# Kernel tuning notes

Measured on AMD Instinct MI355X. Metric: run time of the kernel, lower is better.

The kernel has to match this reference:

```python
import jax, jax.numpy as jnp
import numpy as np
import math

N = 8192  # base points
M = 8192  # target points
FEAT = 5
DESC = 4
HID = 32


def setup_inputs() -> dict:
    key = jax.random.key(0)
    ks = jax.random.split(key, 16)
    s = lambda fan_in: 1.0 / np.sqrt(fan_in)
    return {
        "base_pos": jax.random.normal(ks[0], (N, 2), jnp.float32),
        "base_feat": jax.random.normal(ks[1], (N, FEAT), jnp.float32),
        "base_desc": jax.random.normal(ks[2], (DESC,), jnp.float32),
        "target_pos": jax.random.normal(ks[3], (M, 2), jnp.float32),
        "target_feat": jax.random.normal(ks[4], (M, FEAT), jnp.float32),
        "target_desc": jax.random.normal(ks[5], (DESC,), jnp.float32),
        # NodeWeightNet MLP params (Linear(5,32) -> ReLU -> Linear(32,1))
        "w1": jax.random.uniform(ks[6], (FEAT, HID), jnp.float32, -s(FEAT), s(FEAT)),
        "b1": jax.random.uniform(ks[7], (HID,), jnp.float32, -s(FEAT), s(FEAT)),
        "w2": jax.random.uniform(ks[8], (HID, 1), jnp.float32, -s(HID), s(HID)),
        "b2": jax.random.uniform(ks[9], (1,), jnp.float32, -s(HID), s(HID)),
        # descriptor gate params (Linear(4,32) -> ReLU -> Linear(32,1))
        "g1": jax.random.uniform(ks[10], (DESC, HID), jnp.float32, -s(DESC), s(DESC)),
        "gb1": jax.random.uniform(ks[11], (HID,), jnp.float32, -s(DESC), s(DESC)),
        "g2": jax.random.uniform(ks[12], (HID, 1), jnp.float32, -s(HID), s(HID)),
        "gb2": jax.random.uniform(ks[13], (1,), jnp.float32, -s(HID), s(HID)),
        "log_sigma": jnp.asarray(math.log(0.1), jnp.float32),
        "log_scale": jnp.zeros((2,), jnp.float32),
        "bias": jnp.zeros((1,), jnp.float32),
    }


def _node_weights(feat, w1, b1, w2, b2):
    logits = jax.nn.relu(feat @ w1 + b1) @ w2 + b2  # [N,1]
    w = jax.nn.softplus(logits) + 1e-6
    return (w / w.sum())[:, 0]  # [N], sums to 1


def _mmd_term(x, wx, y, wy, inv_two_sigma2):
    # weighted sum of Gaussian kernel over all pairs, via sq-dist expansion
    d2 = (
        (x * x).sum(-1)[:, None]
        + (y * y).sum(-1)[None, :]
        - 2.0 * (x @ y.T)
    )
    k = jnp.exp(-d2 * inv_two_sigma2)
    return jnp.einsum("i,ij,j->", wx, k, wy)


def reference(base_pos, base_feat, base_desc, target_pos, target_feat, target_desc,
              w1, b1, w2, b2, g1, gb1, g2, gb2, log_sigma, log_scale, bias):
    scale = jnp.exp(log_scale)
    bp = base_pos * scale
    tp = target_pos * scale
    sigma = jnp.exp(log_sigma)
    bw = _node_weights(base_feat, w1, b1, w2, b2)
    tw = _node_weights(target_feat, w1, b1, w2, b2)
    # center=True: subtract each cloud's weighted mean
    bp = bp - (bw[:, None] * bp).sum(0)
    tp = tp - (tw[:, None] * tp).sum(0)
    inv = 1.0 / (2.0 * sigma * sigma)
    loss = (
        _mmd_term(bp, bw, bp, bw, inv)
        - 2.0 * _mmd_term(bp, bw, tp, tw, inv)
        + _mmd_term(tp, tw, tp, tw, inv)
    )
    diff = jnp.abs(base_desc - target_desc)  # [4]
    gate = jax.nn.softplus(jax.nn.relu(diff @ g1 + gb1) @ g2 + gb2) + 1e-6  # [1]
    return loss * gate.squeeze() + bias.squeeze()
```

## Files before the change

kernel.cpp:

```cpp
#include <hip/hip_runtime.h>
#include <math.h>


#define WK_THREADS 256
#define MMD_THREADS 256
#define IB 256
#define JB 256
#define NPART 16

__device__ __forceinline__ float softplusf(float x) {
    return fmaxf(x, 0.0f) + log1pf(expf(-fabsf(x)));
}

__device__ __forceinline__ float fast_exp2(float x) {
#if __has_builtin(__builtin_amdgcn_exp2f)
    return __builtin_amdgcn_exp2f(x);
#else
    return exp2f(x);
#endif
}

__global__ __launch_bounds__(WK_THREADS) void weight_kernel(
    const float* __restrict__ bpos, const float* __restrict__ bfeat,
    const float* __restrict__ tpos, const float* __restrict__ tfeat,
    const float* __restrict__ w1, const float* __restrict__ b1,
    const float* __restrict__ w2, const float* __restrict__ b2,
    const float* __restrict__ log_sigma, const float* __restrict__ log_scale,
    float4* __restrict__ b4, float4* __restrict__ t4,
    float* __restrict__ sums, int n, int m)
{
    int idx = blockIdx.x * WK_THREADS + threadIdx.x;
    int total = n + m;
    float w = 0.f, px = 0.f, py = 0.f;
    int cloud = 0;
    if (idx < total) {
        const float* pos; const float* feat; int i;
        if (idx < n) { pos = bpos; feat = bfeat; i = idx; cloud = 0; }
        else         { pos = tpos; feat = tfeat; i = idx - n; cloud = 1; }
        float sigma = expf(log_sigma[0]);
        float u = 0.8493218003f / sigma;
        float sx = expf(log_scale[0]) * u;
        float sy = expf(log_scale[1]) * u;
        px = pos[2*i]   * sx;
        py = pos[2*i+1] * sy;
        float f0 = feat[5*i], f1 = feat[5*i+1], f2 = feat[5*i+2],
              f3 = feat[5*i+3], f4 = feat[5*i+4];
        float logit = b2[0];
        #pragma unroll
        for (int h = 0; h < 32; ++h) {
            float a = b1[h];
            a = fmaf(f0, w1[h],      a);
            a = fmaf(f1, w1[32+h],   a);
            a = fmaf(f2, w1[64+h],   a);
            a = fmaf(f3, w1[96+h],   a);
            a = fmaf(f4, w1[128+h],  a);
            a = fmaxf(a, 0.f);
            logit = fmaf(a, w2[h], logit);
        }
        w = softplusf(logit) + 1e-6f;
        float4 v = make_float4(px, py, w, 0.f);
        if (cloud == 0) b4[i] = v; else t4[i] = v;
    }
    float sw = w, swx = w*px, swy = w*py;
    #pragma unroll
    for (int off = 32; off > 0; off >>= 1) {
        sw  += __shfl_down(sw,  off, 64);
        swx += __shfl_down(swx, off, 64);
        swy += __shfl_down(swy, off, 64);
    }
    if ((threadIdx.x & 63) == 0 && idx < total) {
        float* dst = sums + 3 + cloud * 3;
        atomicAdd(dst + 0, sw);
        atomicAdd(dst + 1, swx);
        atomicAdd(dst + 2, swy);
    }
}

__global__ __launch_bounds__(MMD_THREADS) void mmd_kernel(
    const float4* __restrict__ b4, const float4* __restrict__ t4,
    const float* __restrict__ sums, float* __restrict__ partial,
    int n, int m)
{
    int t = blockIdx.z;
    const float4* X; const float4* Y; int nx, ny;
    if (t == 0)      { X = b4; Y = b4; nx = n; ny = n; }
    else if (t == 1) { X = b4; Y = t4; nx = n; ny = m; }
    else             { X = t4; Y = t4; nx = m; ny = m; }

    int ibase = blockIdx.x * IB;
    int j0 = blockIdx.y * JB;
    if (ibase >= nx || j0 >= ny) return;

    float dx0 = 0.f, dy0 = 0.f;
    if (t == 1) {
        float sb = sums[3], st = sums[6];
        dx0 = sums[4] / sb - sums[7] / st;
        dy0 = sums[5] / sb - sums[8] / st;
    }

    int i = ibase + threadIdx.x;
    float xi = 0.f, yi = 0.f, wi = 0.f;
    if (i < nx) {
        float4 v = X[i];
        xi = v.x - dx0; yi = v.y - dy0; wi = v.z;
    }

    int jn = min(JB, ny - j0);
    const float4* Yp = Y + j0;
    float acc = 0.f;
    for (int j = 0; j < jn; ++j) {
        float4 q = Yp[j];
        float dx = xi - q.x;
        float dy = yi - q.y;
        float e = fast_exp2(fmaf(dy, -dy, -(dx * dx)));
        acc = fmaf(q.z, e, acc);
    }
    float r = wi * acc;

    #pragma unroll
    for (int off = 32; off > 0; off >>= 1) r += __shfl_down(r, off, 64);
    __shared__ float wsum[MMD_THREADS / 64];
    int wid = threadIdx.x >> 6;
    if ((threadIdx.x & 63) == 0) wsum[wid] = r;
    __syncthreads();
    if (threadIdx.x == 0) {
        float tot = 0.f;
        #pragma unroll
        for (int k = 0; k < MMD_THREADS / 64; ++k) tot += wsum[k];
        atomicAdd(&partial[t * NPART + (blockIdx.x & (NPART - 1))], tot);
    }
}

__global__ void final_kernel(
    const float* __restrict__ bdesc, const float* __restrict__ tdesc,
    const float* __restrict__ g1, const float* __restrict__ gb1,
    const float* __restrict__ g2, const float* __restrict__ gb2,
    const float* __restrict__ bias, const float* __restrict__ sums,
    const float* __restrict__ partial, float* __restrict__ out)
{
    if (threadIdx.x != 0 || blockIdx.x != 0) return;
    float P[3];
    #pragma unroll
    for (int t = 0; t < 3; ++t) {
        float s = 0.f;
        #pragma unroll
        for (int k = 0; k < NPART; ++k) s += partial[t * NPART + k];
        P[t] = s;
    }
    float sb = sums[3], st = sums[6];
    float loss = P[0] / (sb * sb) - 2.f * P[1] / (sb * st) + P[2] / (st * st);

    float d0 = fabsf(bdesc[0] - tdesc[0]);
    float d1 = fabsf(bdesc[1] - tdesc[1]);
    float d2 = fabsf(bdesc[2] - tdesc[2]);
    float d3 = fabsf(bdesc[3] - tdesc[3]);
    float logit = gb2[0];
    #pragma unroll
    for (int h = 0; h < 32; ++h) {
        float a = gb1[h];
        a = fmaf(d0, g1[h],      a);
        a = fmaf(d1, g1[32+h],   a);
        a = fmaf(d2, g1[64+h],   a);
        a = fmaf(d3, g1[96+h],   a);
        a = fmaxf(a, 0.f);
        logit = fmaf(a, g2[h], logit);
    }
    float gate = softplusf(logit) + 1e-6f;
    out[0] = loss * gate + bias[0];
}

extern "C" void kernel_launch(void* const* d_in, const int* in_sizes, int n_in,
                              void* d_out, int out_size, void* d_ws, size_t ws_size,
                              hipStream_t stream)
{
    const float* bpos      = (const float*)d_in[0];
    const float* bfeat     = (const float*)d_in[1];
    const float* bdesc     = (const float*)d_in[2];
    const float* tpos      = (const float*)d_in[3];
    const float* tfeat     = (const float*)d_in[4];
    const float* tdesc     = (const float*)d_in[5];
    const float* w1        = (const float*)d_in[6];
    const float* b1        = (const float*)d_in[7];
    const float* w2        = (const float*)d_in[8];
    const float* b2        = (const float*)d_in[9];
    const float* g1        = (const float*)d_in[10];
    const float* gb1       = (const float*)d_in[11];
    const float* g2        = (const float*)d_in[12];
    const float* gb2       = (const float*)d_in[13];
    const float* log_sigma = (const float*)d_in[14];
    const float* log_scale = (const float*)d_in[15];
    const float* bias      = (const float*)d_in[16];
    float* out = (float*)d_out;

    int n = in_sizes[0] / 2;
    int m = in_sizes[3] / 2;

    char* ws = (char*)d_ws;
    float4* b4   = (float4*)ws;
    float4* t4   = (float4*)(ws + (size_t)n * sizeof(float4));
    float* sums  = (float*)(ws + (size_t)(n + m) * sizeof(float4));
    float* partial = sums + 9;

    hipMemsetAsync(sums, 0, (9 + 3 * NPART) * sizeof(float), stream);

    int total = n + m;
    int wb = (total + WK_THREADS - 1) / WK_THREADS;
    weight_kernel<<<wb, WK_THREADS, 0, stream>>>(
        bpos, bfeat, tpos, tfeat, w1, b1, w2, b2, log_sigma, log_scale,
        b4, t4, sums, n, m);

    int nmax = n > m ? n : m;
    dim3 grid((nmax + IB - 1) / IB, (nmax + JB - 1) / JB, 3);
    mmd_kernel<<<grid, MMD_THREADS, 0, stream>>>(b4, t4, sums, partial, n, m);

    final_kernel<<<1, 64, 0, stream>>>(bdesc, tdesc, g1, gb1, g2, gb2,
                                       bias, sums, partial, out);
}
```

Baseline: 157.4 us.

## Register-block MMD pairs, stage Y tile in LDS, drop atomics and memset

Each MMD thread now handles four i-points against an LDS-staged tile of 128 j-points. The squared distance is expanded as -|x|^2 - |y|^2 + 2x·y, with the per-point norm precomputed in the weight kernel, so each pair costs about three FMAs plus one exp2. Atomic accumulation and the memset are replaced by per-wave and per-block partial slots that are reduced deterministically in the cross-term blocks and in a wider final kernel. The MLP weights are cached in LDS. The trade-off is that every cross-term block redundantly reduces the weight partials, and the expansion form can lose some precision for distant points.

```diff
diff --git a/kernel.cpp b/kernel.cpp
--- a/kernel.cpp
+++ b/kernel.cpp
@@ -4,9 +4,9 @@
 
 #define WK_THREADS 256
 #define MMD_THREADS 256
-#define IB 256
-#define JB 256
-#define NPART 16
+#define I_PT 4
+#define IB (MMD_THREADS * I_PT)
+#define JB 128
 
 __device__ __forceinline__ float softplusf(float x) {
     return fmaxf(x, 0.0f) + log1pf(expf(-fabsf(x)));
@@ -27,9 +27,15 @@
     const float* __restrict__ w2, const float* __restrict__ b2,
     const float* __restrict__ log_sigma, const float* __restrict__ log_scale,
     float4* __restrict__ b4, float4* __restrict__ t4,
-    float* __restrict__ sums, int n, int m)
-{
-    int idx = blockIdx.x * WK_THREADS + threadIdx.x;
+    float* __restrict__ wpart, int n, int m)
+{
+    __shared__ float s_w1[160], s_b1[32], s_w2[32];
+    int tid = threadIdx.x;
+    if (tid < 160) s_w1[tid] = w1[tid];
+    if (tid < 32) { s_b1[tid] = b1[tid]; s_w2[tid] = w2[tid]; }
+    __syncthreads();
+
+    int idx = blockIdx.x * WK_THREADS + tid;
     int total = n + m;
     float w = 0.f, px = 0.f, py = 0.f;
     int cloud = 0;
@@ -48,38 +54,73 @@
         float logit = b2[0];
         #pragma unroll
         for (int h = 0; h < 32; ++h) {
-            float a = b1[h];
-            a = fmaf(f0, w1[h],      a);
-            a = fmaf(f1, w1[32+h],   a);
-            a = fmaf(f2, w1[64+h],   a);
-            a = fmaf(f3, w1[96+h],   a);
-            a = fmaf(f4, w1[128+h],  a);
+            float a = s_b1[h];
+            a = fmaf(f0, s_w1[h],      a);
+            a = fmaf(f1, s_w1[32+h],   a);
+            a = fmaf(f2, s_w1[64+h],   a);
+            a = fmaf(f3, s_w1[96+h],   a);
+            a = fmaf(f4, s_w1[128+h],  a);
             a = fmaxf(a, 0.f);
-            logit = fmaf(a, w2[h], logit);
+            logit = fmaf(a, s_w2[h], logit);
         }
         w = softplusf(logit) + 1e-6f;
-        float4 v = make_float4(px, py, w, 0.f);
+        float h_i = -fmaf(px, px, py * py);
+        float4 v = make_float4(px, py, h_i, w);
         if (cloud == 0) b4[i] = v; else t4[i] = v;
     }
-    float sw = w, swx = w*px, swy = w*py;
+    float sw = w, swx = w * px, swy = w * py;
     #pragma unroll
     for (int off = 32; off > 0; off >>= 1) {
         sw  += __shfl_down(sw,  off, 64);
         swx += __shfl_down(swx, off, 64);
         swy += __shfl_down(swy, off, 64);
     }
-    if ((threadIdx.x & 63) == 0 && idx < total) {
-        float* dst = sums + 3 + cloud * 3;
-        atomicAdd(dst + 0, sw);
-        atomicAdd(dst + 1, swx);
-        atomicAdd(dst + 2, swy);
-    }
+    if ((tid & 63) == 0) {
+        int wgid = blockIdx.x * (WK_THREADS / 64) + (tid >> 6);
+        float* dst = wpart + wgid * 6;
+        bool valid = (idx < total);
+        float z = valid ? 1.f : 0.f;
+        if (cloud == 0) {
+            dst[0] = sw * z; dst[1] = swx * z; dst[2] = swy * z;
+            dst[3] = 0.f;    dst[4] = 0.f;     dst[5] = 0.f;
+        } else {
+            dst[0] = 0.f;    dst[1] = 0.f;     dst[2] = 0.f;
+            dst[3] = sw * z; dst[4] = swx * z; dst[5] = swy * z;
+        }
+    }
+}
+
+__device__ __forceinline__ void reduce_wpart(const float* __restrict__ wpart,
+                                             int nslots, float out[6])
+{
+    __shared__ float lds6[4][6];
+    float v[6];
+    #pragma unroll
+    for (int k = 0; k < 6; ++k) v[k] = 0.f;
+    for (int s = threadIdx.x; s < nslots; s += blockDim.x) {
+        #pragma unroll
+        for (int k = 0; k < 6; ++k) v[k] += wpart[s * 6 + k];
+    }
+    #pragma unroll
+    for (int off = 32; off > 0; off >>= 1) {
+        #pragma unroll
+        for (int k = 0; k < 6; ++k) v[k] += __shfl_down(v[k], off, 64);
+    }
+    if ((threadIdx.x & 63) == 0) {
+        #pragma unroll
+        for (int k = 0; k < 6; ++k) lds6[threadIdx.x >> 6][k] = v[k];
+    }
+    __syncthreads();
+    #pragma unroll
+    for (int k = 0; k < 6; ++k)
+        out[k] = lds6[0][k] + lds6[1][k] + lds6[2][k] + lds6[3][k];
+    __syncthreads();
 }
 
 __global__ __launch_bounds__(MMD_THREADS) void mmd_kernel(
     const float4* __restrict__ b4, const float4* __restrict__ t4,
-    const float* __restrict__ sums, float* __restrict__ partial,
-    int n, int m)
+    const float* __restrict__ wpart, int nwslots,
+    float* __restrict__ partial, int n, int m, int gx, int gy)
 {
     int t = blockIdx.z;
     const float4* X; const float4* Y; int nx, ny;
@@ -87,86 +128,128 @@
     else if (t == 1) { X = b4; Y = t4; nx = n; ny = m; }
     else             { X = t4; Y = t4; nx = m; ny = m; }
 
+    int slot = (t * gy + blockIdx.y) * gx + blockIdx.x;
     int ibase = blockIdx.x * IB;
     int j0 = blockIdx.y * JB;
-    if (ibase >= nx || j0 >= ny) return;
+    if (ibase >= nx || j0 >= ny) {
+        if (threadIdx.x == 0) partial[slot] = 0.f;
+        return;
+    }
 
     float dx0 = 0.f, dy0 = 0.f;
     if (t == 1) {
-        float sb = sums[3], st = sums[6];
-        dx0 = sums[4] / sb - sums[7] / st;
-        dy0 = sums[5] / sb - sums[8] / st;
-    }
-
-    int i = ibase + threadIdx.x;
-    float xi = 0.f, yi = 0.f, wi = 0.f;
-    if (i < nx) {
-        float4 v = X[i];
-        xi = v.x - dx0; yi = v.y - dy0; wi = v.z;
+        float o[6];
+        reduce_wpart(wpart, nwslots, o);
+        dx0 = o[1] / o[0] - o[4] / o[3];
+        dy0 = o[2] / o[0] - o[5] / o[3];
+    }
+
+    __shared__ float4 ytile[JB];
+    if (threadIdx.x < JB) {
+        int jj = j0 + threadIdx.x;
+        ytile[threadIdx.x] = (jj < ny) ? Y[jj] : make_float4(0.f, 0.f, 0.f, 0.f);
+    }
+    __syncthreads();
+
+    float x2[I_PT], y2[I_PT], hi_[I_PT], wi[I_PT], acc[I_PT];
+    #pragma unroll
+    for (int s = 0; s < I_PT; ++s) {
+        int ii = ibase + s * MMD_THREADS + threadIdx.x;
+        float4 v = (ii < nx) ? X[ii] : make_float4(0.f, 0.f, 0.f, 0.f);
+        float xc = v.x - dx0, yc = v.y - dy0;
+        x2[s] = xc + xc;
+        y2[s] = yc + yc;
+        hi_[s] = -fmaf(xc, xc, yc * yc);
+        wi[s] = v.w;
+        acc[s] = 0.f;
     }
 
     int jn = min(JB, ny - j0);
-    const float4* Yp = Y + j0;
-    float acc = 0.f;
+    #pragma unroll 2
     for (int j = 0; j < jn; ++j) {
-        float4 q = Yp[j];
-        float dx = xi - q.x;
-        float dy = yi - q.y;
-        float e = fast_exp2(fmaf(dy, -dy, -(dx * dx)));
-        acc = fmaf(q.z, e, acc);
-    }
-    float r = wi * acc;
+        float4 q = ytile[j];
+        #pragma unroll
+        for (int s = 0; s < I_PT; ++s) {
+            float u = hi_[s] + q.z;
+            u = fmaf(x2[s], q.x, u);
+            u = fmaf(y2[s], q.y, u);
+            acc[s] = fmaf(q.w, fast_exp2(u), acc[s]);
+        }
+    }
+    float r = 0.f;
+    #pragma unroll
+    for (int s = 0; s < I_PT; ++s) r = fmaf(wi[s], acc[s], r);
 
     #pragma unroll
     for (int off = 32; off > 0; off >>= 1) r += __shfl_down(r, off, 64);
     __shared__ float wsum[MMD_THREADS / 64];
-    int wid = threadIdx.x >> 6;
-    if ((threadIdx.x & 63) == 0) wsum[wid] = r;
+    if ((threadIdx.x & 63) == 0) wsum[threadIdx.x >> 6] = r;
     __syncthreads();
     if (threadIdx.x == 0) {
         float tot = 0.f;
         #pragma unroll
         for (int k = 0; k < MMD_THREADS / 64; ++k) tot += wsum[k];
-        atomicAdd(&partial[t * NPART + (blockIdx.x & (NPART - 1))], tot);
-    }
-}
-
-__global__ void final_kernel(
+        partial[slot] = tot;
+    }
+}
+
+__global__ __launch_bounds__(256) void final_kernel(
     const float* __restrict__ bdesc, const float* __restrict__ tdesc,
     const float* __restrict__ g1, const float* __restrict__ gb1,
     const float* __restrict__ g2, const float* __restrict__ gb2,
-    const float* __restrict__ bias, const float* __restrict__ sums,
-    const float* __restrict__ partial, float* __restrict__ out)
-{
-    if (threadIdx.x != 0 || blockIdx.x != 0) return;
-    float P[3];
-    #pragma unroll
-    for (int t = 0; t < 3; ++t) {
-        float s = 0.f;
-        #pragma unroll
-        for (int k = 0; k < NPART; ++k) s += partial[t * NPART + k];
-        P[t] = s;
-    }
-    float sb = sums[3], st = sums[6];
-    float loss = P[0] / (sb * sb) - 2.f * P[1] / (sb * st) + P[2] / (st * st);
-
-    float d0 = fabsf(bdesc[0] - tdesc[0]);
-    float d1 = fabsf(bdesc[1] - tdesc[1]);
-    float d2 = fabsf(bdesc[2] - tdesc[2]);
-    float d3 = fabsf(bdesc[3] - tdesc[3]);
-    float logit = gb2[0];
-    #pragma unroll
-    for (int h = 0; h < 32; ++h) {
-        float a = gb1[h];
-        a = fmaf(d0, g1[h],      a);
-        a = fmaf(d1, g1[32+h],   a);
-        a = fmaf(d2, g1[64+h],   a);
-        a = fmaf(d3, g1[96+h],   a);
-        a = fmaxf(a, 0.f);
-        logit = fmaf(a, g2[h], logit);
-    }
-    float gate = softplusf(logit) + 1e-6f;
-    out[0] = loss * gate + bias[0];
+    const float* __restrict__ bias, const float* __restrict__ wpart, int nwslots,
+    const float* __restrict__ partial, int gx, int gy,
+    float* __restrict__ out)
+{
+    float o[6];
+    reduce_wpart(wpart, nwslots, o);
+    float sb = o[0], st = o[3];
+
+    int np1 = gx * gy;
+    float p0 = 0.f, p1 = 0.f, p2 = 0.f;
+    for (int k = threadIdx.x; k < 3 * np1; k += 256) {
+        float v = partial[k];
+        int term = k / np1;
+        if (term == 0) p0 += v; else if (term == 1) p1 += v; else p2 += v;
+    }
+    #pragma unroll
+    for (int off = 32; off > 0; off >>= 1) {
+        p0 += __shfl_down(p0, off, 64);
+        p1 += __shfl_down(p1, off, 64);
+        p2 += __shfl_down(p2, off, 64);
+    }
+    __shared__ float lds3[4][3];
+    if ((threadIdx.x & 63) == 0) {
+        lds3[threadIdx.x >> 6][0] = p0;
+        lds3[threadIdx.x >> 6][1] = p1;
+        lds3[threadIdx.x >> 6][2] = p2;
+    }
+    __syncthreads();
+    float P0 = lds3[0][0] + lds3[1][0] + lds3[2][0] + lds3[3][0];
+    float P1 = lds3[0][1] + lds3[1][1] + lds3[2][1] + lds3[3][1];
+    float P2 = lds3[0][2] + lds3[1][2] + lds3[2][2] + lds3[3][2];
+
+    float a = 0.f;
+    if (threadIdx.x < 32) {
+        int h = threadIdx.x;
+        float d0 = fabsf(bdesc[0] - tdesc[0]);
+        float d1 = fabsf(bdesc[1] - tdesc[1]);
+        float d2 = fabsf(bdesc[2] - tdesc[2]);
+        float d3 = fabsf(bdesc[3] - tdesc[3]);
+        float v = gb1[h];
+        v = fmaf(d0, g1[h],      v);
+        v = fmaf(d1, g1[32+h],   v);
+        v = fmaf(d2, g1[64+h],   v);
+        v = fmaf(d3, g1[96+h],   v);
+        a = fmaxf(v, 0.f) * g2[h];
+    }
+    #pragma unroll
+    for (int off = 16; off > 0; off >>= 1) a += __shfl_down(a, off, 64);
+    if (threadIdx.x == 0) {
+        float gate = softplusf(a + gb2[0]) + 1e-6f;
+        float loss = P0 / (sb * sb) - 2.f * P1 / (sb * st) + P2 / (st * st);
+        out[0] = loss * gate + bias[0];
+    }
 }
 
 extern "C" void kernel_launch(void* const* d_in, const int* in_sizes, int n_in,
@@ -195,24 +278,27 @@
     int n = in_sizes[0] / 2;
     int m = in_sizes[3] / 2;
 
+    int wb = (n + m + WK_THREADS - 1) / WK_THREADS;
+    int nwslots = wb * (WK_THREADS / 64);
+    int nmax = n > m ? n : m;
+    int gx = (nmax + IB - 1) / IB;
+    int gy = (nmax + JB - 1) / JB;
+
     char* ws = (char*)d_ws;
-    float4* b4   = (float4*)ws;
-    float4* t4   = (float4*)(ws + (size_t)n * sizeof(float4));
-    float* sums  = (float*)(ws + (size_t)(n + m) * sizeof(float4));
-    float* partial = sums + 9;
-
-    hipMemsetAsync(sums, 0, (9 + 3 * NPART) * sizeof(float), stream);
-
-    int total = n + m;
-    int wb = (total + WK_THREADS - 1) / WK_THREADS;
+    float4* b4    = (float4*)ws;
+    float4* t4    = (float4*)(ws + (size_t)n * sizeof(float4));
+    float* wpart  = (float*)(ws + (size_t)(n + m) * sizeof(float4));
+    float* partial = wpart + (size_t)nwslots * 6;
+
     weight_kernel<<<wb, WK_THREADS, 0, stream>>>(
         bpos, bfeat, tpos, tfeat, w1, b1, w2, b2, log_sigma, log_scale,
-        b4, t4, sums, n, m);
-
-    int nmax = n > m ? n : m;
-    dim3 grid((nmax + IB - 1) / IB, (nmax + JB - 1) / JB, 3);
-    mmd_kernel<<<grid, MMD_THREADS, 0, stream>>>(b4, t4, sums, partial, n, m);
-
-    final_kernel<<<1, 64, 0, stream>>>(bdesc, tdesc, g1, gb1, g2, gb2,
-                                       bias, sums, partial, out);
-}
+        b4, t4, wpart, n, m);
+
+    dim3 grid(gx, gy, 3);
+    mmd_kernel<<<grid, MMD_THREADS, 0, stream>>>(
+        b4, t4, wpart, nwslots, partial, n, m, gx, gy);
+
+    final_kernel<<<1, 256, 0, stream>>>(
+        bdesc, tdesc, g1, gb1, g2, gb2, bias, wpart, nwslots,
+        partial, gx, gy, out);
+}
```

New measurement: 126.5 us. -19.7%, faster.
